# Performance work log

Measured on AMD Instinct MI355X. Metric: run time of the kernel, lower is better.

## Reference

```python
import jax, jax.numpy as jnp
import numpy as np

DIM = 768
HEADS = 12
DIM_HEAD = 64
INNER = HEADS * DIM_HEAD
L = 256
EPS = 1e-08


def setup_inputs() -> dict:
    key = jax.random.key(0)
    k1, k2, k3, k4 = jax.random.split(key, 4)
    x = jax.random.normal(k1, (2, 4096, DIM), dtype=jnp.float32)
    # Linear weights stored torch-style: (out_features, in_features)
    w_qkv = jax.random.normal(k2, (3 * INNER, DIM), dtype=jnp.float32) * (DIM ** -0.5)
    w_out = jax.random.normal(k3, (DIM, INNER), dtype=jnp.float32) * (INNER ** -0.5)
    b_out = jax.random.normal(k4, (DIM,), dtype=jnp.float32) * 0.01
    # learned per-head log-scale temperature, init log2(L^2 - L)
    scale = jnp.full((HEADS,), np.log2(L * L - L), dtype=jnp.float32)
    return {"x": x, "w_qkv": w_qkv, "w_out": w_out, "b_out": b_out, "scale": scale}


def reference(x, w_qkv, w_out, b_out, scale):
    b, n, d = x.shape
    h, dh = HEADS, DIM_HEAD
    qkv = x @ w_qkv.T                                   # [b, n, 3*inner]
    q, k, v = jnp.split(qkv, 3, axis=-1)
    # [b, n, h, dh] -> [b, h, n, dh]
    q, k, v = (t.reshape(b, n, h, dh).transpose(0, 2, 1, 3) for t in (q, k, v))
    # Faithful to source: L2 norm over the HEADS axis (dim=1), then rsqrt
    q = q * jax.lax.rsqrt(jnp.linalg.norm(q, axis=1, keepdims=True) + EPS)
    k = k * jax.lax.rsqrt(jnp.linalg.norm(k, axis=1, keepdims=True) + EPS)
    dots = jnp.einsum('bhid,bhjd->bhij', q, k)          # [b, h, n, n]
    scores = jax.nn.softmax(dots / scale[:, None, None], axis=-1)
    out = jnp.einsum('bhij,bhjd->bhid', scores, v)      # [b, h, n, dh]
    out = out.transpose(0, 2, 1, 3).reshape(b, n, h * dh)
    return out @ w_out.T + b_out
```

## Files before the change

### kernel.cpp

```cpp
#include <hip/hip_runtime.h>
#include <hip/hip_bf16.h>

#define DIMX   768
#define HEADS  12
#define DH     64
#define INNER  768
#define NQKV   2304
#define SEQ    4096
#define BATCH  2
#define ROWS   (BATCH*SEQ)
#define EPSF   1e-8f
#define LOG2E  1.4426950408889634f

typedef __bf16 bf16x8 __attribute__((ext_vector_type(8)));
typedef float  f32x4  __attribute__((ext_vector_type(4)));
typedef float  f32x16 __attribute__((ext_vector_type(16)));

__device__ __forceinline__ unsigned short f2bf(float f) {
    unsigned int u = __float_as_uint(f);
    unsigned int r = ((u >> 16) & 1u) + 0x7FFFu;
    return (unsigned short)((u + r) >> 16);
}
__device__ __forceinline__ float bf2f(unsigned short u) {
    return __builtin_bit_cast(float, (unsigned)u << 16);
}
__device__ __forceinline__ unsigned pkbf(float a, float b) {
    unsigned short la = __builtin_bit_cast(unsigned short, (__bf16)a);
    unsigned short lb = __builtin_bit_cast(unsigned short, (__bf16)b);
    return (unsigned)la | ((unsigned)lb << 16);
}

__global__ __launch_bounds__(256) void cast_f32_bf16(
    const float* __restrict__ src, unsigned short* __restrict__ dst, int n)
{
    int i = (blockIdx.x * 256 + threadIdx.x) * 4;
    if (i + 3 < n) {
        float4 v = *reinterpret_cast<const float4*>(src + i);
        ushort4 o;
        o.x = f2bf(v.x); o.y = f2bf(v.y); o.z = f2bf(v.z); o.w = f2bf(v.w);
        *reinterpret_cast<ushort4*>(dst + i) = o;
    }
}

template<bool BF16OUT>
__global__ __launch_bounds__(256) void gemm_bt_kernel(
    const unsigned short* __restrict__ A,
    const unsigned short* __restrict__ B,
    void* __restrict__ Cv,
    const float* __restrict__ bias,
    int M, int N, int K)
{
    __shared__ unsigned short shA[128][72];
    __shared__ unsigned short shB[128][72];

    const int bm0 = blockIdx.x * 128;
    const int bn0 = blockIdx.y * 128;
    const int tid = threadIdx.x;
    const int lane = tid & 63;
    const int wid  = tid >> 6;
    const int l15  = lane & 15;
    const int l4   = lane >> 4;
    const int wr   = wid >> 1;
    const int wc   = wid & 1;

    f32x4 acc[4][4];
    #pragma unroll
    for (int i = 0; i < 4; ++i)
        #pragma unroll
        for (int j = 0; j < 4; ++j)
            acc[i][j] = (f32x4){0.f, 0.f, 0.f, 0.f};

    const int nkt = K >> 6;
    for (int kt = 0; kt < nkt; ++kt) {
        const int k0 = kt << 6;
        __syncthreads();
        #pragma unroll
        for (int it = 0; it < 4; ++it) {
            int c = tid + it * 256;
            int row = c >> 3, colc = c & 7;
            *reinterpret_cast<uint4*>(&shA[row][colc * 8]) =
                *reinterpret_cast<const uint4*>(&A[(size_t)(bm0 + row) * K + k0 + colc * 8]);
            *reinterpret_cast<uint4*>(&shB[row][colc * 8]) =
                *reinterpret_cast<const uint4*>(&B[(size_t)(bn0 + row) * K + k0 + colc * 8]);
        }
        __syncthreads();
        #pragma unroll
        for (int ks = 0; ks < 2; ++ks) {
            bf16x8 af[4], bfr[4];
            #pragma unroll
            for (int mf = 0; mf < 4; ++mf)
                af[mf] = *reinterpret_cast<const bf16x8*>(&shA[wr * 64 + mf * 16 + l15][ks * 32 + l4 * 8]);
            #pragma unroll
            for (int nf = 0; nf < 4; ++nf)
                bfr[nf] = *reinterpret_cast<const bf16x8*>(&shB[wc * 64 + nf * 16 + l15][ks * 32 + l4 * 8]);
            #pragma unroll
            for (int mf = 0; mf < 4; ++mf)
                #pragma unroll
                for (int nf = 0; nf < 4; ++nf)
                    acc[mf][nf] = __builtin_amdgcn_mfma_f32_16x16x32_bf16(
                        af[mf], bfr[nf], acc[mf][nf], 0, 0, 0);
        }
    }

    #pragma unroll
    for (int mf = 0; mf < 4; ++mf) {
        #pragma unroll
        for (int nf = 0; nf < 4; ++nf) {
            int col = bn0 + wc * 64 + nf * 16 + l15;
            float badd = bias ? bias[col] : 0.f;
            #pragma unroll
            for (int r = 0; r < 4; ++r) {
                int row = bm0 + wr * 64 + mf * 16 + l4 * 4 + r;
                if constexpr (BF16OUT)
                    ((unsigned short*)Cv)[(size_t)row * N + col] = f2bf(acc[mf][nf][r] + badd);
                else
                    ((float*)Cv)[(size_t)row * N + col] = acc[mf][nf][r] + badd;
            }
        }
    }
}

__global__ __launch_bounds__(256) void normalize_kernel(
    const unsigned short* __restrict__ qkv,
    const float* __restrict__ scale,
    unsigned short* __restrict__ qo,
    unsigned short* __restrict__ ko)
{
    int t = blockIdx.x * 256 + threadIdx.x;
    int row = t >> 6;
    int d = t & 63;
    int b = row >> 12;
    int n = row & 4095;
    const unsigned short* base = qkv + (size_t)row * NQKV;

    float qv[12], kv[12];
    float sq = 0.f, sk = 0.f;
    #pragma unroll
    for (int h = 0; h < 12; ++h) {
        qv[h] = bf2f(base[h * 64 + d]);
        kv[h] = bf2f(base[768 + h * 64 + d]);
        sq += qv[h] * qv[h];
        sk += kv[h] * kv[h];
    }
    float rq = rsqrtf(sqrtf(sq) + EPSF);
    float rk = rsqrtf(sqrtf(sk) + EPSF);
    #pragma unroll
    for (int h = 0; h < 12; ++h) {
        size_t bh = (size_t)(b * 12 + h);
        float fold = LOG2E / scale[h];
        qo[(bh * SEQ + n) * 64 + d] = f2bf(qv[h] * rq * fold);
        ko[(bh * SEQ + n) * 64 + d] = f2bf(kv[h] * rk);
    }
}

__global__ __launch_bounds__(256) void vtrans_kernel(
    const unsigned short* __restrict__ qkv,
    unsigned short* __restrict__ vt)
{
    __shared__ unsigned short tile[64][72];
    const int bh = blockIdx.x;
    const int nt = blockIdx.y;
    const int b = bh / HEADS, h = bh % HEADS;
    const int tid = threadIdx.x;

    #pragma unroll
    for (int it = 0; it < 2; ++it) {
        int c = tid + it * 256;
        int r = c >> 3, cc = c & 7;
        *reinterpret_cast<uint4*>(&tile[r][cc * 8]) =
            *reinterpret_cast<const uint4*>(
                &qkv[(size_t)(b * SEQ + nt * 64 + r) * NQKV + 1536 + h * 64 + cc * 8]);
    }
    __syncthreads();
    #pragma unroll
    for (int it = 0; it < 2; ++it) {
        int c = tid + it * 256;
        int d = c >> 3, nc = c & 7;
        ushort4 o0, o1;
        o0.x = tile[nc * 8 + 0][d]; o0.y = tile[nc * 8 + 1][d];
        o0.z = tile[nc * 8 + 2][d]; o0.w = tile[nc * 8 + 3][d];
        o1.x = tile[nc * 8 + 4][d]; o1.y = tile[nc * 8 + 5][d];
        o1.z = tile[nc * 8 + 6][d]; o1.w = tile[nc * 8 + 7][d];
        unsigned short* dst = &vt[((size_t)bh * 64 + d) * SEQ + nt * 64 + nc * 8];
        *reinterpret_cast<ushort4*>(dst)     = o0;
        *reinterpret_cast<ushort4*>(dst + 4) = o1;
    }
}

__global__ __launch_bounds__(256) void attn_kernel(
    const unsigned short* __restrict__ qg,
    const unsigned short* __restrict__ kg,
    const unsigned short* __restrict__ vtg,
    unsigned short* __restrict__ attnout)
{
    __shared__ unsigned short shK[64][72];
    __shared__ unsigned short shV[64][72];

    const int qblk = blockIdx.x;
    const int bh   = blockIdx.y;
    const int b    = bh / HEADS;
    const int h    = bh % HEADS;
    const int tid  = threadIdx.x;
    const int lane = tid & 63;
    const int wid  = tid >> 6;
    const int l31  = lane & 31;
    const int hi   = lane >> 5;

    bf16x8 qf[4];
    {
        const unsigned short* qrow =
            qg + ((size_t)bh * SEQ + qblk * 128 + wid * 32 + l31) * 64 + hi * 8;
        #pragma unroll
        for (int d0 = 0; d0 < 4; ++d0)
            qf[d0] = *reinterpret_cast<const bf16x8*>(qrow + d0 * 16);
    }

    f32x16 ot[2];
    #pragma unroll
    for (int r = 0; r < 16; ++r) { ot[0][r] = 0.f; ot[1][r] = 0.f; }
    float l_lane = 0.f;

    const unsigned short* kbase = kg  + (size_t)bh * SEQ * 64;
    const unsigned short* vbase = vtg + (size_t)bh * 64 * SEQ;

    for (int kt = 0; kt < SEQ / 64; ++kt) {
        __syncthreads();
        #pragma unroll
        for (int it = 0; it < 2; ++it) {
            int c = tid + it * 256;
            int row = c >> 3, colc = c & 7;
            *reinterpret_cast<uint4*>(&shK[row][colc * 8]) =
                *reinterpret_cast<const uint4*>(&kbase[(size_t)(kt * 64 + row) * 64 + colc * 8]);
            *reinterpret_cast<uint4*>(&shV[row][colc * 8]) =
                *reinterpret_cast<const uint4*>(&vbase[(size_t)row * SEQ + kt * 64 + colc * 8]);
        }
        __syncthreads();

        f32x16 st0, st1;
        #pragma unroll
        for (int r = 0; r < 16; ++r) { st0[r] = 0.f; st1[r] = 0.f; }
        #pragma unroll
        for (int d0 = 0; d0 < 4; ++d0) {
            bf16x8 kf0 = *reinterpret_cast<const bf16x8*>(&shK[l31][d0 * 16 + hi * 8]);
            bf16x8 kf1 = *reinterpret_cast<const bf16x8*>(&shK[32 + l31][d0 * 16 + hi * 8]);
            st0 = __builtin_amdgcn_mfma_f32_32x32x16_bf16(kf0, qf[d0], st0, 0, 0, 0);
            st1 = __builtin_amdgcn_mfma_f32_32x32x16_bf16(kf1, qf[d0], st1, 0, 0, 0);
        }

        float s0 = 0.f, s1 = 0.f, s2 = 0.f, s3 = 0.f;
        unsigned cp0[8], cp1[8];
        #pragma unroll
        for (int t = 0; t < 8; ++t) {
            float pa = __builtin_amdgcn_exp2f(st0[2 * t]);
            float pb = __builtin_amdgcn_exp2f(st0[2 * t + 1]);
            float pc = __builtin_amdgcn_exp2f(st1[2 * t]);
            float pd = __builtin_amdgcn_exp2f(st1[2 * t + 1]);
            s0 += pa; s1 += pb; s2 += pc; s3 += pd;
            cp0[t] = pkbf(pa, pb);
            cp1[t] = pkbf(pc, pd);
        }
        l_lane += (s0 + s1) + (s2 + s3);

        #pragma unroll
        for (int cb = 0; cb < 2; ++cb) {
            #pragma unroll
            for (int kk = 0; kk < 2; ++kk) {
                unsigned c0 = cb ? cp1[4 * kk + 0] : cp0[4 * kk + 0];
                unsigned c1 = cb ? cp1[4 * kk + 1] : cp0[4 * kk + 1];
                unsigned c2 = cb ? cp1[4 * kk + 2] : cp0[4 * kk + 2];
                unsigned c3 = cb ? cp1[4 * kk + 3] : cp0[4 * kk + 3];
                unsigned e0 = __shfl_xor(c0, 32);
                unsigned e1 = __shfl_xor(c1, 32);
                unsigned e2 = __shfl_xor(c2, 32);
                unsigned e3 = __shfl_xor(c3, 32);
                union { unsigned uu[4]; bf16x8 v; } pu;
                pu.uu[0] = hi ? e2 : c0;
                pu.uu[1] = hi ? e3 : c1;
                pu.uu[2] = hi ? c2 : e0;
                pu.uu[3] = hi ? c3 : e1;
                #pragma unroll
                for (int df = 0; df < 2; ++df) {
                    bf16x8 vf = *reinterpret_cast<const bf16x8*>(
                        &shV[df * 32 + l31][cb * 32 + kk * 16 + hi * 8]);
                    ot[df] = __builtin_amdgcn_mfma_f32_32x32x16_bf16(vf, pu.v, ot[df], 0, 0, 0);
                }
            }
        }
    }

    float l_all = l_lane + __shfl_xor(l_lane, 32);
    float invl = 1.0f / l_all;
    int n = qblk * 128 + wid * 32 + l31;
    unsigned short* orow = attnout + ((size_t)(b * SEQ + n)) * INNER + h * 64;
    #pragma unroll
    for (int df = 0; df < 2; ++df) {
        #pragma unroll
        for (int t = 0; t < 4; ++t) {
            unsigned w0 = pkbf(ot[df][4 * t]     * invl, ot[df][4 * t + 1] * invl);
            unsigned w1 = pkbf(ot[df][4 * t + 2] * invl, ot[df][4 * t + 3] * invl);
            unsigned long long pk = (unsigned long long)w0 | ((unsigned long long)w1 << 32);
            *reinterpret_cast<unsigned long long*>(orow + df * 32 + t * 8 + hi * 4) = pk;
        }
    }
}

extern "C" void kernel_launch(void* const* d_in, const int* in_sizes, int n_in,
                              void* d_out, int out_size, void* d_ws, size_t ws_size,
                              hipStream_t stream)
{
    const float* x      = (const float*)d_in[0];
    const float* w_qkv  = (const float*)d_in[1];
    const float* w_out  = (const float*)d_in[2];
    const float* b_out  = (const float*)d_in[3];
    const float* scale  = (const float*)d_in[4];
    float* out = (float*)d_out;
    char* ws = (char*)d_ws;

    unsigned short* xb    = (unsigned short*)(ws);
    unsigned short* wqkvb = (unsigned short*)(ws + 12582912);
    unsigned short* woutb = (unsigned short*)(ws + 16121856);
    unsigned short* attnb = (unsigned short*)(ws + 17301504);
    unsigned short* qb    = (unsigned short*)(ws + 29884416);
    unsigned short* kb    = (unsigned short*)(ws + 42467328);
    unsigned short* vtb   = (unsigned short*)(ws + 55050240);
    unsigned short* qkvb  = (unsigned short*)(ws + 67633152);

    cast_f32_bf16<<<6144, 256, 0, stream>>>(x, xb, 6291456);
    cast_f32_bf16<<<1728, 256, 0, stream>>>(w_qkv, wqkvb, 1769472);
    cast_f32_bf16<<<576, 256, 0, stream>>>(w_out, woutb, 589824);

    gemm_bt_kernel<true><<<dim3(64, 18), 256, 0, stream>>>(xb, wqkvb, qkvb, nullptr, ROWS, NQKV, DIMX);

    normalize_kernel<<<2048, 256, 0, stream>>>(qkvb, scale, qb, kb);
    vtrans_kernel<<<dim3(BATCH * HEADS, SEQ / 64), 256, 0, stream>>>(qkvb, vtb);

    attn_kernel<<<dim3(SEQ / 128, BATCH * HEADS), 256, 0, stream>>>(qb, kb, vtb, attnb);

    gemm_bt_kernel<false><<<dim3(64, 6), 256, 0, stream>>>(attnb, woutb, out, b_out, ROWS, INNER, INNER);
}
```

Measured before the change: 254.0 us.

## Split attention KV range into two partial passes plus combine kernel

```diff
diff --git a/kernel.cpp b/kernel.cpp
--- a/kernel.cpp
+++ b/kernel.cpp
@@ -191,15 +191,15 @@
     const unsigned short* __restrict__ qg,
     const unsigned short* __restrict__ kg,
     const unsigned short* __restrict__ vtg,
-    unsigned short* __restrict__ attnout)
+    float* __restrict__ po,
+    float* __restrict__ pl)
 {
     __shared__ unsigned short shK[64][72];
     __shared__ unsigned short shV[64][72];
 
     const int qblk = blockIdx.x;
     const int bh   = blockIdx.y;
-    const int b    = bh / HEADS;
-    const int h    = bh % HEADS;
+    const int g    = blockIdx.z;
     const int tid  = threadIdx.x;
     const int lane = tid & 63;
     const int wid  = tid >> 6;
@@ -220,10 +220,10 @@
     for (int r = 0; r < 16; ++r) { ot[0][r] = 0.f; ot[1][r] = 0.f; }
     float l_lane = 0.f;
 
-    const unsigned short* kbase = kg  + (size_t)bh * SEQ * 64;
-    const unsigned short* vbase = vtg + (size_t)bh * 64 * SEQ;
-
-    for (int kt = 0; kt < SEQ / 64; ++kt) {
+    const unsigned short* kbase = kg  + ((size_t)bh * SEQ + g * 2048) * 64;
+    const unsigned short* vbase = vtg + (size_t)bh * 64 * SEQ + g * 2048;
+
+    for (int kt = 0; kt < 32; ++kt) {
         __syncthreads();
         #pragma unroll
         for (int it = 0; it < 2; ++it) {
@@ -289,19 +289,49 @@
     }
 
     float l_all = l_lane + __shfl_xor(l_lane, 32);
-    float invl = 1.0f / l_all;
     int n = qblk * 128 + wid * 32 + l31;
-    unsigned short* orow = attnout + ((size_t)(b * SEQ + n)) * INNER + h * 64;
+    float* prow = po + ((size_t)(g * 24 + bh) * SEQ + n) * 64;
     #pragma unroll
     for (int df = 0; df < 2; ++df) {
         #pragma unroll
         for (int t = 0; t < 4; ++t) {
-            unsigned w0 = pkbf(ot[df][4 * t]     * invl, ot[df][4 * t + 1] * invl);
-            unsigned w1 = pkbf(ot[df][4 * t + 2] * invl, ot[df][4 * t + 3] * invl);
-            unsigned long long pk = (unsigned long long)w0 | ((unsigned long long)w1 << 32);
-            *reinterpret_cast<unsigned long long*>(orow + df * 32 + t * 8 + hi * 4) = pk;
-        }
-    }
+            float4 v = make_float4(ot[df][4 * t], ot[df][4 * t + 1],
+                                   ot[df][4 * t + 2], ot[df][4 * t + 3]);
+            *reinterpret_cast<float4*>(prow + df * 32 + t * 8 + hi * 4) = v;
+        }
+    }
+    if (hi == 0)
+        pl[(size_t)(g * 24 + bh) * SEQ + n] = l_all;
+}
+
+__global__ __launch_bounds__(256) void combine_kernel(
+    const float* __restrict__ po,
+    const float* __restrict__ pl,
+    unsigned short* __restrict__ attnout)
+{
+    int idx = blockIdx.x * 256 + threadIdx.x;
+    int oct = idx & 7;
+    int q   = (idx >> 3) & 4095;
+    int bh  = idx >> 15;
+    int b = bh / HEADS, h = bh % HEADS;
+    int d0 = oct * 8;
+
+    size_t base = ((size_t)bh * SEQ + q) * 64 + d0;
+    const float* p0 = po + base;
+    const float* p1 = po + (size_t)24 * SEQ * 64 + base;
+    float4 a0 = *reinterpret_cast<const float4*>(p0);
+    float4 a1 = *reinterpret_cast<const float4*>(p0 + 4);
+    float4 b0 = *reinterpret_cast<const float4*>(p1);
+    float4 b1 = *reinterpret_cast<const float4*>(p1 + 4);
+    float l = pl[(size_t)bh * SEQ + q] + pl[(size_t)24 * SEQ + bh * SEQ + q];
+    float inv = 1.0f / l;
+
+    unsigned w0 = pkbf((a0.x + b0.x) * inv, (a0.y + b0.y) * inv);
+    unsigned w1 = pkbf((a0.z + b0.z) * inv, (a0.w + b0.w) * inv);
+    unsigned w2 = pkbf((a1.x + b1.x) * inv, (a1.y + b1.y) * inv);
+    unsigned w3 = pkbf((a1.z + b1.z) * inv, (a1.w + b1.w) * inv);
+    uint4 ov = make_uint4(w0, w1, w2, w3);
+    *reinterpret_cast<uint4*>(&attnout[((size_t)(b * SEQ + q)) * INNER + h * 64 + d0]) = ov;
 }
 
 extern "C" void kernel_launch(void* const* d_in, const int* in_sizes, int n_in,
@@ -324,6 +354,8 @@
     unsigned short* kb    = (unsigned short*)(ws + 42467328);
     unsigned short* vtb   = (unsigned short*)(ws + 55050240);
     unsigned short* qkvb  = (unsigned short*)(ws + 67633152);
+    float*          po    = (float*)(ws + 67633152);
+    float*          pl    = (float*)(ws + 117964800);
 
     cast_f32_bf16<<<6144, 256, 0, stream>>>(x, xb, 6291456);
     cast_f32_bf16<<<1728, 256, 0, stream>>>(w_qkv, wqkvb, 1769472);
@@ -334,7 +366,8 @@
     normalize_kernel<<<2048, 256, 0, stream>>>(qkvb, scale, qb, kb);
     vtrans_kernel<<<dim3(BATCH * HEADS, SEQ / 64), 256, 0, stream>>>(qkvb, vtb);
 
-    attn_kernel<<<dim3(SEQ / 128, BATCH * HEADS), 256, 0, stream>>>(qb, kb, vtb, attnb);
+    attn_kernel<<<dim3(SEQ / 128, BATCH * HEADS, 2), 256, 0, stream>>>(qb, kb, vtb, po, pl);
+    combine_kernel<<<3072, 256, 0, stream>>>(po, pl, attnb);
 
     gemm_bt_kernel<false><<<dim3(64, 6), 256, 0, stream>>>(attnb, woutb, out, b_out, ROWS, INNER, INNER);
 }
```

Result: slower. 263.8 us (+3.9%).

## Double-buffer K/V tiles in attention and use direct global-to-LDS loads in GEMM

Applied to the files above, without the earlier changes.

```diff
diff --git a/kernel.cpp b/kernel.cpp
--- a/kernel.cpp
+++ b/kernel.cpp
@@ -30,6 +30,12 @@
     return (unsigned)la | ((unsigned)lb << 16);
 }
 
+__device__ __forceinline__ void gload_lds16(const void* g, void* l) {
+    __builtin_amdgcn_global_load_lds(
+        (const __attribute__((address_space(1))) void*)g,
+        (__attribute__((address_space(3))) void*)l, 16, 0, 0);
+}
+
 __global__ __launch_bounds__(256) void cast_f32_bf16(
     const float* __restrict__ src, unsigned short* __restrict__ dst, int n)
 {
@@ -50,8 +56,8 @@
     const float* __restrict__ bias,
     int M, int N, int K)
 {
-    __shared__ unsigned short shA[128][72];
-    __shared__ unsigned short shB[128][72];
+    __shared__ unsigned short shA[128][64];
+    __shared__ unsigned short shB[128][64];
 
     const int bm0 = blockIdx.x * 128;
     const int bn0 = blockIdx.y * 128;
@@ -62,6 +68,8 @@
     const int l4   = lane >> 4;
     const int wr   = wid >> 1;
     const int wc   = wid & 1;
+    const int srow = lane >> 3;
+    const int scol = (lane & 7) * 8;
 
     f32x4 acc[4][4];
     #pragma unroll
@@ -75,13 +83,10 @@
         const int k0 = kt << 6;
         __syncthreads();
         #pragma unroll
-        for (int it = 0; it < 4; ++it) {
-            int c = tid + it * 256;
-            int row = c >> 3, colc = c & 7;
-            *reinterpret_cast<uint4*>(&shA[row][colc * 8]) =
-                *reinterpret_cast<const uint4*>(&A[(size_t)(bm0 + row) * K + k0 + colc * 8]);
-            *reinterpret_cast<uint4*>(&shB[row][colc * 8]) =
-                *reinterpret_cast<const uint4*>(&B[(size_t)(bn0 + row) * K + k0 + colc * 8]);
+        for (int j = 0; j < 4; ++j) {
+            int row = wid * 32 + j * 8;
+            gload_lds16(&A[(size_t)(bm0 + row + srow) * K + k0 + scol], &shA[row][0]);
+            gload_lds16(&B[(size_t)(bn0 + row + srow) * K + k0 + scol], &shB[row][0]);
         }
         __syncthreads();
         #pragma unroll
@@ -193,8 +198,8 @@
     const unsigned short* __restrict__ vtg,
     unsigned short* __restrict__ attnout)
 {
-    __shared__ unsigned short shK[64][72];
-    __shared__ unsigned short shV[64][72];
+    __shared__ unsigned short shK[2][64][72];
+    __shared__ unsigned short shV[2][64][72];
 
     const int qblk = blockIdx.x;
     const int bh   = blockIdx.y;
@@ -205,6 +210,8 @@
     const int wid  = tid >> 6;
     const int l31  = lane & 31;
     const int hi   = lane >> 5;
+    const int r0 = tid >> 3;
+    const int sc = (tid & 7) * 8;
 
     bf16x8 qf[4];
     {
@@ -223,26 +230,35 @@
     const unsigned short* kbase = kg  + (size_t)bh * SEQ * 64;
     const unsigned short* vbase = vtg + (size_t)bh * 64 * SEQ;
 
+    uint4 rk0 = *reinterpret_cast<const uint4*>(&kbase[(size_t)r0 * 64 + sc]);
+    uint4 rk1 = *reinterpret_cast<const uint4*>(&kbase[(size_t)(32 + r0) * 64 + sc]);
+    uint4 rv0 = *reinterpret_cast<const uint4*>(&vbase[(size_t)r0 * SEQ + sc]);
+    uint4 rv1 = *reinterpret_cast<const uint4*>(&vbase[(size_t)(32 + r0) * SEQ + sc]);
+    *reinterpret_cast<uint4*>(&shK[0][r0][sc])      = rk0;
+    *reinterpret_cast<uint4*>(&shK[0][32 + r0][sc]) = rk1;
+    *reinterpret_cast<uint4*>(&shV[0][r0][sc])      = rv0;
+    *reinterpret_cast<uint4*>(&shV[0][32 + r0][sc]) = rv1;
+
     for (int kt = 0; kt < SEQ / 64; ++kt) {
+        const int cur = kt & 1;
         __syncthreads();
-        #pragma unroll
-        for (int it = 0; it < 2; ++it) {
-            int c = tid + it * 256;
-            int row = c >> 3, colc = c & 7;
-            *reinterpret_cast<uint4*>(&shK[row][colc * 8]) =
-                *reinterpret_cast<const uint4*>(&kbase[(size_t)(kt * 64 + row) * 64 + colc * 8]);
-            *reinterpret_cast<uint4*>(&shV[row][colc * 8]) =
-                *reinterpret_cast<const uint4*>(&vbase[(size_t)row * SEQ + kt * 64 + colc * 8]);
-        }
-        __syncthreads();
+
+        if (kt < SEQ / 64 - 1) {
+            const unsigned short* kn = kbase + (size_t)(kt + 1) * 64 * 64;
+            const unsigned short* vn = vbase + (size_t)(kt + 1) * 64;
+            rk0 = *reinterpret_cast<const uint4*>(&kn[(size_t)r0 * 64 + sc]);
+            rk1 = *reinterpret_cast<const uint4*>(&kn[(size_t)(32 + r0) * 64 + sc]);
+            rv0 = *reinterpret_cast<const uint4*>(&vn[(size_t)r0 * SEQ + sc]);
+            rv1 = *reinterpret_cast<const uint4*>(&vn[(size_t)(32 + r0) * SEQ + sc]);
+        }
 
         f32x16 st0, st1;
         #pragma unroll
         for (int r = 0; r < 16; ++r) { st0[r] = 0.f; st1[r] = 0.f; }
         #pragma unroll
         for (int d0 = 0; d0 < 4; ++d0) {
-            bf16x8 kf0 = *reinterpret_cast<const bf16x8*>(&shK[l31][d0 * 16 + hi * 8]);
-            bf16x8 kf1 = *reinterpret_cast<const bf16x8*>(&shK[32 + l31][d0 * 16 + hi * 8]);
+            bf16x8 kf0 = *reinterpret_cast<const bf16x8*>(&shK[cur][l31][d0 * 16 + hi * 8]);
+            bf16x8 kf1 = *reinterpret_cast<const bf16x8*>(&shK[cur][32 + l31][d0 * 16 + hi * 8]);
             st0 = __builtin_amdgcn_mfma_f32_32x32x16_bf16(kf0, qf[d0], st0, 0, 0, 0);
             st1 = __builtin_amdgcn_mfma_f32_32x32x16_bf16(kf1, qf[d0], st1, 0, 0, 0);
         }
@@ -281,10 +297,17 @@
                 #pragma unroll
                 for (int df = 0; df < 2; ++df) {
                     bf16x8 vf = *reinterpret_cast<const bf16x8*>(
-                        &shV[df * 32 + l31][cb * 32 + kk * 16 + hi * 8]);
+                        &shV[cur][df * 32 + l31][cb * 32 + kk * 16 + hi * 8]);
                     ot[df] = __builtin_amdgcn_mfma_f32_32x32x16_bf16(vf, pu.v, ot[df], 0, 0, 0);
                 }
             }
+        }
+
+        if (kt < SEQ / 64 - 1) {
+            *reinterpret_cast<uint4*>(&shK[cur ^ 1][r0][sc])      = rk0;
+            *reinterpret_cast<uint4*>(&shK[cur ^ 1][32 + r0][sc]) = rk1;
+            *reinterpret_cast<uint4*>(&shV[cur ^ 1][r0][sc])      = rv0;
+            *reinterpret_cast<uint4*>(&shV[cur ^ 1][32 + r0][sc]) = rv1;
         }
     }
 
```

Measured after the change: 276.4 us. 8.8% more time.
